# Optimization experiments

Hardware: AMD Instinct MI355X
Metric: run time of the kernel (lower is better)

Reference implementation:

```python
import jax, jax.numpy as jnp
import numpy as np
import math

BATCH, SEQ, DIM, HEADS = 2, 2048, 1024, 16
HD = DIM // HEADS  # 64
HID = int(DIM * 4 * 2 / 3)  # 2730


def cosine_norm(x):
    n = jnp.maximum(jnp.linalg.norm(x, axis=-1, keepdims=True), 1e-6)
    return x / n


def make_freqs(seq_len, head_dim, theta=10000.0):
    inv_freq = 1.0 / theta ** (jnp.arange(0, head_dim, 2, dtype=jnp.float32) / head_dim)
    t = jnp.arange(seq_len, dtype=jnp.float32)
    f = t[:, None] * inv_freq[None, :]            # [S, HD/2]
    emb = jnp.concatenate([f, f], axis=-1)        # [S, HD]
    return jnp.cos(emb)[None, :, None, :], jnp.sin(emb)[None, :, None, :]


def apply_rope(x, sin, cos):
    # x: [B, S, H, HD]
    x_real = x * cos
    x1, x2 = jnp.split(x, 2, axis=-1)
    x_imag = jnp.concatenate([-x2, x1], axis=-1) * sin
    return x_real + x_imag


def setup_inputs() -> dict:
    key = jax.random.key(0)
    ks = jax.random.split(key, 9)
    std = 0.02
    return {
        "x": jax.random.normal(ks[0], (BATCH, SEQ, DIM), dtype=jnp.float32),
        "Wq": jax.random.normal(ks[1], (DIM, DIM), dtype=jnp.float32) * std,
        "Wk": jax.random.normal(ks[2], (DIM, DIM), dtype=jnp.float32) * std,
        "Wv": jax.random.normal(ks[3], (DIM, DIM), dtype=jnp.float32) * std,
        "Wo": jax.random.normal(ks[4], (DIM, DIM), dtype=jnp.float32) * std,
        "s_qk": jnp.ones((HEADS, HD), dtype=jnp.float32) / math.sqrt(DIM),
        "a_A": jnp.ones((DIM,), dtype=jnp.float32) / math.sqrt(DIM),
        "Wup": jax.random.normal(ks[5], (DIM, HID), dtype=jnp.float32) * std,
        "Wgate": jax.random.normal(ks[6], (DIM, HID), dtype=jnp.float32) * std,
        "Wdown": jax.random.normal(ks[7], (HID, DIM), dtype=jnp.float32) * std,
        "s_u": jnp.ones((HID,), dtype=jnp.float32),
        "s_v": jnp.ones((HID,), dtype=jnp.float32),
        "a_M": jnp.ones((DIM,), dtype=jnp.float32) / math.sqrt(DIM),
    }


def attention(x, Wq, Wk, Wv, Wo, s_qk, cos, sin, mask):
    B, S, _ = x.shape
    q = (x @ Wq).reshape(B, S, HEADS, HD)
    k = (x @ Wk).reshape(B, S, HEADS, HD)
    v = (x @ Wv).reshape(B, S, HEADS, HD)
    q = apply_rope(q, sin, cos)
    k = apply_rope(k, sin, cos)
    eff_s_qk = s_qk * math.sqrt(DIM)  # s_qk_init / s_qk_scale = sqrt(dim)
    q = cosine_norm(q) * eff_s_qk
    k = cosine_norm(k) * eff_s_qk
    logits = jnp.einsum("bqhd,bkhd->bhqk", q, k) * math.sqrt(HD)
    logits = jnp.where(mask, logits, -jnp.inf)
    probs = jax.nn.softmax(logits, axis=-1)
    out = jnp.einsum("bhqk,bkhd->bqhd", probs, v).reshape(B, S, DIM)
    return out @ Wo


def mlp(x, Wup, Wgate, Wdown, s_u, s_v):
    u = (x @ Wup) * s_u                          # s_u_init/s_u_scale = 1
    v = (x @ Wgate) * s_v * math.sqrt(DIM)       # scale = sqrt(input_dim)
    return (u * jax.nn.silu(v)) @ Wdown


def reference(x, Wq, Wk, Wv, Wo, s_qk, a_A, Wup, Wgate, Wdown, s_u, s_v, a_M):
    cos, sin = make_freqs(SEQ, HD)
    mask = jnp.tril(jnp.ones((SEQ, SEQ), dtype=bool))[None, None, :, :]
    h = x
    h_A = cosine_norm(attention(h, Wq, Wk, Wv, Wo, s_qk, cos, sin, mask))
    h = cosine_norm(h + a_A * (h_A - h))
    h_M = cosine_norm(mlp(h, Wup, Wgate, Wdown, s_u, s_v))
    h = cosine_norm(h + a_M * (h_M - h))
    return h
```

## Files before the change

kernel.cpp:

```cpp
#include <hip/hip_runtime.h>
#include <math.h>

#define DEVI __device__ __forceinline__

typedef __attribute__((ext_vector_type(4))) float f32x4;
typedef __attribute__((ext_vector_type(8))) short bf16x8;

DEVI short f2bf(float f) {
    union { float f; unsigned u; } v; v.f = f;
    unsigned r = v.u + 0x7fffu + ((v.u >> 16) & 1u);
    return (short)(r >> 16);
}
DEVI float bf2f(short s) {
    union { unsigned u; float f; } v; v.u = ((unsigned)(unsigned short)s) << 16;
    return v.f;
}

DEVI f32x4 mfma16(bf16x8 a, bf16x8 b, f32x4 c) {
    return __builtin_amdgcn_mfma_f32_16x16x32_bf16(a, b, c, 0, 0, 0);
}

DEVI void gload16(const short* g, short* l) {
    __builtin_amdgcn_global_load_lds((__attribute__((address_space(1))) void*)(g),
                                     (__attribute__((address_space(3))) void*)(l),
                                     16, 0, 0);
}

DEVI void trans_tile(const float* in, short* out, int R, int C, int Rpad, int Cpad,
                     int rmul, int radd, int bx, int by) {
    __shared__ float tile[32][33];
    int c0 = bx * 32, r0 = by * 32;
    int tx = threadIdx.x & 31, ty = threadIdx.x >> 5;
#pragma unroll
    for (int i = 0; i < 4; i++) {
        int r = r0 + ty + 8 * i, c = c0 + tx;
        tile[ty + 8 * i][tx] = (r < R && c < C) ? in[(size_t)r * C + c] : 0.0f;
    }
    __syncthreads();
#pragma unroll
    for (int i = 0; i < 4; i++) {
        int oc = c0 + ty + 8 * i;
        int orr = r0 + tx;
        if (oc < Cpad && orr < Rpad)
            out[(size_t)(oc * rmul + radd) * Rpad + orr] = f2bf(tile[tx][ty + 8 * i]);
    }
}

__global__ void k_prep(const float* __restrict__ x, short* __restrict__ xbf,
                       float* __restrict__ cost, float* __restrict__ sint,
                       const float* __restrict__ Wq, const float* __restrict__ Wk,
                       const float* __restrict__ Wv, const float* __restrict__ Wo,
                       const float* __restrict__ Wup, const float* __restrict__ Wg,
                       const float* __restrict__ Wd,
                       short* __restrict__ wqkvT, short* __restrict__ woT,
                       short* __restrict__ wugT, short* __restrict__ wdownT) {
    int b = blockIdx.x;
    if (b < 4096) {
        int i = (b * 256 + threadIdx.x) * 4;
        float4 v = *(const float4*)(x + i);
        short4 o;
        o.x = f2bf(v.x); o.y = f2bf(v.y); o.z = f2bf(v.z); o.w = f2bf(v.w);
        *(short4*)(xbf + i) = o;
    } else if (b < 4352) {
        int i = (b - 4096) * 256 + threadIdx.x;
        int s = i >> 5, j = i & 31;
        double inv = pow(10000.0, -(double)j / 32.0);
        double f = (double)s * inv;
        cost[i] = (float)cos(f);
        sint[i] = (float)sin(f);
    } else {
        int bb = b - 4352;
        if (bb < 4096) {
            int seg = bb >> 10, idx = bb & 1023;
            const float* in = seg == 0 ? Wq : seg == 1 ? Wk : seg == 2 ? Wv : Wo;
            short* out = seg == 0 ? wqkvT : seg == 1 ? wqkvT + 1048576
                       : seg == 2 ? wqkvT + 2097152 : woT;
            trans_tile(in, out, 1024, 1024, 1024, 1024, 1, 0, idx & 31, idx >> 5);
        } else if (bb < 9600) {
            int idx = bb - 4096;
            int seg = idx >= 2752;
            idx -= seg * 2752;
            trans_tile(seg ? Wg : Wup, wugT, 1024, 2730, 1024, 2752, 2, seg, idx % 86, idx / 86);
        } else {
            int idx = bb - 9600;
            trans_tile(Wd, wdownT, 2730, 1024, 2752, 1024, 1, 0, idx & 31, idx >> 5);
        }
    }
}

template <int EPI>
__launch_bounds__(256, 4)
__global__ void k_gemm128(const short* __restrict__ A, const short* __restrict__ BT,
                          void* __restrict__ Cv, void* __restrict__ Cv1,
                          int M, int N, int K, int nkblk, int nsplit,
                          const float* __restrict__ s_u, const float* __restrict__ s_v,
                          const float* __restrict__ cost, const float* __restrict__ sint,
                          const float* __restrict__ sqk,
                          short* __restrict__ qn, short* __restrict__ kn,
                          short* __restrict__ vtout) {
    __shared__ __align__(16) short As[128 * 64];
    __shared__ __align__(16) short Bs[128 * 64];
    const int t = threadIdx.x;
    const int w = t >> 6;
    const int lane = t & 63;
    const int lr = lane & 15, lg = lane >> 4;
    const int nwg = (int)gridDim.x;
    int wg = ((int)blockIdx.x & 7) * (nwg >> 3) + ((int)blockIdx.x >> 3);
    int half = 0;
    if (nsplit == 2) {
        const int per = nwg >> 1;
        half = wg >= per;
        wg -= half * per;
    }
    const int MT = M >> 7;
    const int m0 = (wg % MT) << 7;
    const int n0 = (wg / MT) << 7;
    const int koff = half * nkblk * 64;
    const int ntile = (nsplit == 2 && half) ? (K >> 6) - nkblk : nkblk;
    const int wr = (w >> 1) * 64, wc = (w & 1) * 64;

    const int srow = t >> 3;
    const int scol = (((t & 7) ^ (srow & 7)) << 3);
    const short* Ap = A + (size_t)(m0 + srow) * K + koff + scol;
    const short* Bp = BT + (size_t)(n0 + srow) * K + koff + scol;
    const size_t rstep = (size_t)32 * K;
    const int dW = (w * 8) * 64;

    const int ca = (wr + lr) & 7;
    const int cb = (wc + lr) & 7;
    const short* pa0 = &As[(wr + lr) * 64 + (((0 + lg) ^ ca) << 3)];
    const short* pa1 = &As[(wr + lr) * 64 + (((4 + lg) ^ ca) << 3)];
    const short* pb0 = &Bs[(wc + lr) * 64 + (((0 + lg) ^ cb) << 3)];
    const short* pb1 = &Bs[(wc + lr) * 64 + (((4 + lg) ^ cb) << 3)];

    f32x4 acc[4][4];
#pragma unroll
    for (int m = 0; m < 4; m++)
#pragma unroll
        for (int n = 0; n < 4; n++)
            acc[m][n] = (f32x4){0.f, 0.f, 0.f, 0.f};

    for (int kt = 0; kt < ntile; kt++) {
        if (kt) __syncthreads();
#pragma unroll
        for (int j = 0; j < 4; j++) {
            gload16(Ap + j * rstep, As + dW + j * 2048);
            gload16(Bp + j * rstep, Bs + dW + j * 2048);
        }
        Ap += 64; Bp += 64;
        __syncthreads();
#pragma unroll
        for (int ks = 0; ks < 2; ks++) {
            const short* pa = ks ? pa1 : pa0;
            const short* pb = ks ? pb1 : pb0;
            bf16x8 af[4], bfr[4];
#pragma unroll
            for (int m = 0; m < 4; m++)
                af[m] = *(const bf16x8*)(pa + m * 1024);
#pragma unroll
            for (int n = 0; n < 4; n++)
                bfr[n] = *(const bf16x8*)(pb + n * 1024);
#pragma unroll
            for (int m = 0; m < 4; m++)
#pragma unroll
                for (int n = 0; n < 4; n++)
                    acc[m][n] = mfma16(af[m], bfr[n], acc[m][n]);
        }
    }

    if (EPI == 3) {
        const int sector = n0 >> 10;
        if (sector == 2) {
#pragma unroll
            for (int m = 0; m < 4; m++)
#pragma unroll
                for (int n = 0; n < 4; n++) {
                    int col = n0 + wc + n * 16 + lr - 2048;
                    int hh = col >> 6, d = col & 63;
                    int brow = m0 + wr + m * 16 + lg * 4;
                    int bb = brow >> 11, s = brow & 2047;
                    short4 o4;
                    o4.x = f2bf(acc[m][n][0]); o4.y = f2bf(acc[m][n][1]);
                    o4.z = f2bf(acc[m][n][2]); o4.w = f2bf(acc[m][n][3]);
                    *(short4*)&vtout[((size_t)((bb * 16 + hh) * 64 + d)) * 2048 + s] = o4;
                }
        } else {
            const int h = ((n0 + wc) >> 6) & 15;
            float eff[4];
#pragma unroll
            for (int n = 0; n < 4; n++)
                eff[n] = sqk[h * 64 + n * 16 + lr] * 32.0f;
            short* dst = (sector == 0) ? qn : kn;
            const float extra = (sector == 0) ? 8.0f : 1.0f;
#pragma unroll
            for (int m = 0; m < 4; m++)
#pragma unroll
                for (int i = 0; i < 4; i++) {
                    int row = m0 + wr + m * 16 + lg * 4 + i;
                    int b = row >> 11, s = row & 2047;
                    float cs0 = cost[s * 32 + lr],      sn0 = sint[s * 32 + lr];
                    float cs1 = cost[s * 32 + 16 + lr], sn1 = sint[s * 32 + 16 + lr];
                    float vr0 = acc[m][0][i] * cs0 - acc[m][2][i] * sn0;
                    float vr1 = acc[m][1][i] * cs1 - acc[m][3][i] * sn1;
                    float vr2 = acc[m][2][i] * cs0 + acc[m][0][i] * sn0;
                    float vr3 = acc[m][3][i] * cs1 + acc[m][1][i] * sn1;
                    float ss = vr0 * vr0 + vr1 * vr1 + vr2 * vr2 + vr3 * vr3;
#pragma unroll
                    for (int o = 1; o < 16; o <<= 1)
                        ss += __shfl_xor(ss, o, 64);
                    float sc = extra / fmaxf(sqrtf(ss), 1e-6f);
                    size_t base = ((size_t)(b * 16 + h) * 2048 + s) * 64;
                    dst[base + lr]      = f2bf(vr0 * eff[0] * sc);
                    dst[base + 16 + lr] = f2bf(vr1 * eff[1] * sc);
                    dst[base + 32 + lr] = f2bf(vr2 * eff[2] * sc);
                    dst[base + 48 + lr] = f2bf(vr3 * eff[3] * sc);
                }
        }
        return;
    }

#pragma unroll
    for (int m = 0; m < 4; m++)
#pragma unroll
        for (int n = 0; n < 4; n++) {
            int row = m0 + wr + m * 16 + lg * 4;
            int col = n0 + wc + n * 16 + lr;
            if (EPI == 2) {
                int j = col >> 1;
                int jc = j < 2730 ? j : 2729;
                float su = s_u[jc];
                float sg = s_v[jc] * 32.0f;
#pragma unroll
                for (int i = 0; i < 4; i++) {
                    float own = acc[m][n][i];
                    float oth = __shfl_xor(own, 1, 64);
                    float u = (lr & 1) ? oth : own;
                    float g = (lr & 1) ? own : oth;
                    float uu = u * su;
                    float vv = g * sg;
                    float wv = uu * vv / (1.0f + expf(-vv));
                    if (!(lr & 1))
                        ((short*)Cv)[(size_t)(row + i) * (N >> 1) + j] = f2bf(wv);
                }
            } else {
                void* outp = half ? Cv1 : Cv;
#pragma unroll
                for (int i = 0; i < 4; i++) {
                    if (EPI == 1)
                        ((short*)outp)[(size_t)(row + i) * N + col] = f2bf(acc[m][n][i]);
                    else
                        ((float*)outp)[(size_t)(row + i) * N + col] = acc[m][n][i];
                }
            }
        }
}

__launch_bounds__(512)
__global__ void k_attn(const short* __restrict__ qn, const short* __restrict__ kn,
                       const short* __restrict__ vt, short* __restrict__ opart,
                       float* __restrict__ lsump) {
    __shared__ __align__(16) short Ks[2][64 * 64];
    __shared__ __align__(16) short Vs[2][64 * 64];
    __shared__ __align__(16) short Ps[8][32 * 64];
    const int t = threadIdx.x;
    const int w = t >> 6, lane = t & 63;
    const int bid = blockIdx.x;
    const int xcd = bid & 7, idx = bid >> 3;
    const int bhg = xcd + ((idx >> 3) << 3);
    const int pslot = idx & 7;
    const int h = bhg & 15, b = bhg >> 4;
    const int bh = b * 16 + h;
    const int lr = lane & 15, lg = lane >> 4;
    const short* Qb = qn + (size_t)bh * 2048 * 64;
    const short* Kb = kn + (size_t)bh * 2048 * 64;
    const short* Vb = vt + (size_t)bh * 64 * 2048;
    char* pwc = (char*)&Ps[w][0];

#define STAGE_KV(bi, kbase)                                                          \
    {                                                                                \
        int row = w * 8 + (lane >> 3);                                               \
        int scol = (lane & 7) ^ (row & 7);                                           \
        gload16(Kb + (size_t)((kbase) + row) * 64 + scol * 8,                        \
                &Ks[bi][(w * 8) * 64]);                                              \
        gload16(Vb + (size_t)row * 2048 + (kbase) + scol * 8,                        \
                &Vs[bi][(w * 8) * 64]);                                              \
    }

    for (int pc = 0; pc < 2; pc++) {
        const int qb = pc == 0 ? pslot : 7 - pslot;
        const int hf = pc;
        const int ktn = 2 * qb + 2;
        const int kt0 = hf * ktn, kt1 = kt0 + ktn;
        const int qw = qb * 256 + w * 32;

        bf16x8 qf[2][2];
#pragma unroll
        for (int mi = 0; mi < 2; mi++)
#pragma unroll
            for (int kk = 0; kk < 2; kk++)
                qf[mi][kk] = *(const bf16x8*)&Qb[(size_t)(qw + mi * 16 + lr) * 64 + kk * 32 + lg * 8];

        f32x4 oacc[2][4];
#pragma unroll
        for (int mi = 0; mi < 2; mi++)
#pragma unroll
            for (int ct = 0; ct < 4; ct++) oacc[mi][ct] = (f32x4){0.f, 0.f, 0.f, 0.f};
        float psum[2][4];
#pragma unroll
        for (int mi = 0; mi < 2; mi++)
#pragma unroll
            for (int i = 0; i < 4; i++) psum[mi][i] = 0.0f;

        if (pc) __syncthreads();
        STAGE_KV(0, kt0 << 6);

        for (int kt = kt0; kt < kt1; kt++) {
            const int kbase = kt << 6;
            const int cur = (kt - kt0) & 1;
            __syncthreads();
            if (kt + 1 < kt1) STAGE_KV(cur ^ 1, (kt + 1) << 6);

            bf16x8 kf[4][2];
#pragma unroll
            for (int ni = 0; ni < 4; ni++)
#pragma unroll
                for (int kk = 0; kk < 2; kk++) {
                    int row = ni * 16 + lr;
                    kf[ni][kk] = *(const bf16x8*)&Ks[cur][row * 64 + (((kk * 4 + lg) ^ (row & 7)) << 3)];
                }
            f32x4 sv[2][4];
#pragma unroll
            for (int mi = 0; mi < 2; mi++)
#pragma unroll
                for (int ni = 0; ni < 4; ni++) {
                    f32x4 s = (f32x4){0.f, 0.f, 0.f, 0.f};
                    s = mfma16(qf[mi][0], kf[ni][0], s);
                    s = mfma16(qf[mi][1], kf[ni][1], s);
                    sv[mi][ni] = s;
                }
            if (kbase + 63 > qw) {
#pragma unroll
                for (int mi = 0; mi < 2; mi++)
#pragma unroll
                    for (int ni = 0; ni < 4; ni++)
#pragma unroll
                        for (int i = 0; i < 4; i++) {
                            int qg = qw + mi * 16 + lg * 4 + i;
                            int kg = kbase + ni * 16 + lr;
                            if (kg > qg) sv[mi][ni][i] = -3.0e38f;
                        }
            }
#pragma unroll
            for (int mi = 0; mi < 2; mi++) {
#pragma unroll
                for (int ni = 0; ni < 4; ni++)
#pragma unroll
                    for (int i = 0; i < 4; i++) {
                        float p = exp2f((sv[mi][ni][i] - 9.0f) * 1.44269504f);
                        sv[mi][ni][i] = p;
                        psum[mi][i] += p;
                    }
#pragma unroll
                for (int ni = 0; ni < 4; ni++)
#pragma unroll
                    for (int i = 0; i < 4; i++) {
                        int row = mi * 16 + lg * 4 + i;
                        int col = ni * 16 + lr;
                        unsigned off = (unsigned)(row * 128 + col * 2) ^ ((unsigned)(row & 7) << 4);
                        *(short*)(pwc + off) = f2bf(sv[mi][ni][i]);
                    }
            }
            bf16x8 pa[2][2];
#pragma unroll
            for (int mi = 0; mi < 2; mi++)
#pragma unroll
                for (int kk = 0; kk < 2; kk++) {
                    int row = mi * 16 + lr;
                    unsigned off = (unsigned)(row * 128 + kk * 64 + lg * 16) ^ ((unsigned)(row & 7) << 4);
                    pa[mi][kk] = *(const bf16x8*)(pwc + off);
                }
            bf16x8 vf[4][2];
#pragma unroll
            for (int ct = 0; ct < 4; ct++)
#pragma unroll
                for (int kk = 0; kk < 2; kk++) {
                    int row = ct * 16 + lr;
                    vf[ct][kk] = *(const bf16x8*)&Vs[cur][row * 64 + (((kk * 4 + lg) ^ (row & 7)) << 3)];
                }
#pragma unroll
            for (int mi = 0; mi < 2; mi++)
#pragma unroll
                for (int ct = 0; ct < 4; ct++) {
                    oacc[mi][ct] = mfma16(pa[mi][0], vf[ct][0], oacc[mi][ct]);
                    oacc[mi][ct] = mfma16(pa[mi][1], vf[ct][1], oacc[mi][ct]);
                }
        }

#pragma unroll
        for (int o = 1; o < 16; o <<= 1)
#pragma unroll
            for (int mi = 0; mi < 2; mi++)
#pragma unroll
                for (int i = 0; i < 4; i++)
                    psum[mi][i] += __shfl_xor(psum[mi][i], o, 64);

        short* aob = opart + (size_t)hf * 4096 * 1024 + ((size_t)(b * 2048 + qw) * 1024) + h * 64;
#pragma unroll
        for (int mi = 0; mi < 2; mi++)
#pragma unroll
            for (int ct = 0; ct < 4; ct++)
#pragma unroll
                for (int i = 0; i < 4; i++) {
                    int q = mi * 16 + lg * 4 + i;
                    aob[(size_t)q * 1024 + ct * 16 + lr] = f2bf(oacc[mi][ct][i]);
                }
        if (lr == 0) {
#pragma unroll
            for (int mi = 0; mi < 2; mi++)
#pragma unroll
                for (int i = 0; i < 4; i++)
                    lsump[hf * 65536 + bh * 2048 + qw + mi * 16 + lg * 4 + i] = psum[mi][i];
        }
    }
#undef STAGE_KV
}

__global__ void k_comb(const short* __restrict__ op, const float* __restrict__ ls,
                       short* __restrict__ ao) {
    int i = (blockIdx.x * 256 + threadIdx.x) * 4;
    int row = i >> 10, col = i & 1023;
    int idx = ((row >> 11) * 16 + (col >> 6)) * 2048 + (row & 2047);
    float rl = 1.0f / (ls[idx] + ls[65536 + idx]);
    short4 a = *(const short4*)(op + i);
    short4 c = *(const short4*)(op + 4194304 + i);
    short4 o;
    o.x = f2bf((bf2f(a.x) + bf2f(c.x)) * rl);
    o.y = f2bf((bf2f(a.y) + bf2f(c.y)) * rl);
    o.z = f2bf((bf2f(a.z) + bf2f(c.z)) * rl);
    o.w = f2bf((bf2f(a.w) + bf2f(c.w)) * rl);
    *(short4*)(ao + i) = o;
}

__global__ void k_resnorm(const float* base, const short* __restrict__ pre0,
                          const short* __restrict__ pre1,
                          const float* __restrict__ alpha, float* outf,
                          short* __restrict__ outb) {
    __shared__ float red1[4], red2[4];
    int row = blockIdx.x;
    int t = threadIdx.x;
    int w = t >> 6;
    float4 p;
    short4 a = *(const short4*)(pre0 + (size_t)row * 1024 + t * 4);
    short4 c = *(const short4*)(pre1 + (size_t)row * 1024 + t * 4);
    p.x = bf2f(a.x) + bf2f(c.x); p.y = bf2f(a.y) + bf2f(c.y);
    p.z = bf2f(a.z) + bf2f(c.z); p.w = bf2f(a.w) + bf2f(c.w);
    float ss = p.x * p.x + p.y * p.y + p.z * p.z + p.w * p.w;
#pragma unroll
    for (int o = 1; o < 64; o <<= 1) ss += __shfl_xor(ss, o, 64);
    if ((t & 63) == 0) red1[w] = ss;
    __syncthreads();
    float inv1 = 1.0f / fmaxf(sqrtf(red1[0] + red1[1] + red1[2] + red1[3]), 1e-6f);
    const float4 bx = *(const float4*)(base + (size_t)row * 1024 + t * 4);
    const float4 av = *(const float4*)(alpha + t * 4);
    float4 tm;
    tm.x = bx.x + av.x * (p.x * inv1 - bx.x);
    tm.y = bx.y + av.y * (p.y * inv1 - bx.y);
    tm.z = bx.z + av.z * (p.z * inv1 - bx.z);
    tm.w = bx.w + av.w * (p.w * inv1 - bx.w);
    float ss2 = tm.x * tm.x + tm.y * tm.y + tm.z * tm.z + tm.w * tm.w;
#pragma unroll
    for (int o = 1; o < 64; o <<= 1) ss2 += __shfl_xor(ss2, o, 64);
    if ((t & 63) == 0) red2[w] = ss2;
    __syncthreads();
    float inv2 = 1.0f / fmaxf(sqrtf(red2[0] + red2[1] + red2[2] + red2[3]), 1e-6f);
    float4 hv;
    hv.x = tm.x * inv2; hv.y = tm.y * inv2; hv.z = tm.z * inv2; hv.w = tm.w * inv2;
    if (outf) *(float4*)(outf + (size_t)row * 1024 + t * 4) = hv;
    if (outb) {
        short4 o4;
        o4.x = f2bf(hv.x); o4.y = f2bf(hv.y); o4.z = f2bf(hv.z); o4.w = f2bf(hv.w);
        *(short4*)(outb + (size_t)row * 1024 + t * 4) = o4;
    }
}

extern "C" void kernel_launch(void* const* d_in, const int* in_sizes, int n_in,
                              void* d_out, int out_size, void* d_ws, size_t ws_size,
                              hipStream_t stream) {
    (void)in_sizes; (void)n_in; (void)out_size; (void)ws_size;
    const float* x   = (const float*)d_in[0];
    const float* Wq  = (const float*)d_in[1];
    const float* Wk  = (const float*)d_in[2];
    const float* Wv  = (const float*)d_in[3];
    const float* Wo  = (const float*)d_in[4];
    const float* sqk = (const float*)d_in[5];
    const float* aA  = (const float*)d_in[6];
    const float* Wup = (const float*)d_in[7];
    const float* Wg  = (const float*)d_in[8];
    const float* Wd  = (const float*)d_in[9];
    const float* su  = (const float*)d_in[10];
    const float* sv  = (const float*)d_in[11];
    const float* aM  = (const float*)d_in[12];

    char* ws = (char*)d_ws;
    short* wqkvT  = (short*)(ws + 0);
    short* woT    = (short*)(ws + 6291456);
    short* wugT   = (short*)(ws + 8388608);
    short* wdownT = (short*)(ws + 19660800);
    float* cost   = (float*)(ws + 25296896);
    float* sint   = (float*)(ws + 25559040);
    short* xbf    = (short*)(ws + 25821184);
    short* qn     = (short*)(ws + 34209792);
    short* kn     = (short*)(ws + 42598400);
    short* vt     = (short*)(ws + 50987008);
    short* opart  = (short*)(ws + 59375616);
    float* lsum   = (float*)(ws + 25296896);
    short* ao     = (short*)(ws + 34209792);
    short* hA0    = (short*)(ws + 42598400);
    short* hA1    = (short*)(ws + 50987008);
    float* h1f    = (float*)d_out;
    short* h1bf   = (short*)(ws + 25821184);
    short* wmlp   = (short*)(ws + 34209792);
    short* hM0    = (short*)(ws + 59375616);
    short* hM1    = (short*)(ws + 67764224);

    k_prep<<<16704, 256, 0, stream>>>(x, xbf, cost, sint, Wq, Wk, Wv, Wo, Wup, Wg, Wd,
                                      wqkvT, woT, wugT, wdownT);

    k_gemm128<3><<<768, 256, 0, stream>>>(xbf, wqkvT, nullptr, nullptr, 4096, 3072, 1024,
                                          16, 1, nullptr, nullptr, cost, sint, sqk, qn, kn, vt);
    k_attn<<<256, 512, 0, stream>>>(qn, kn, vt, opart, lsum);
    k_comb<<<4096, 256, 0, stream>>>(opart, lsum, ao);
    k_gemm128<1><<<512, 256, 0, stream>>>(ao, woT, hA0, hA1, 4096, 1024, 1024,
                                          8, 2, nullptr, nullptr, nullptr, nullptr, nullptr,
                                          nullptr, nullptr, nullptr);
    k_resnorm<<<4096, 256, 0, stream>>>(x, hA0, hA1, aA, h1f, h1bf);
    k_gemm128<2><<<1376, 256, 0, stream>>>(h1bf, wugT, wmlp, nullptr, 4096, 5504, 1024,
                                           16, 1, su, sv, nullptr, nullptr, nullptr,
                                           nullptr, nullptr, nullptr);
    k_gemm128<1><<<512, 256, 0, stream>>>(wmlp, wdownT, hM0, hM1, 4096, 1024, 2752,
                                          22, 2, nullptr, nullptr, nullptr, nullptr, nullptr,
                                          nullptr, nullptr, nullptr);
    k_resnorm<<<4096, 256, 0, stream>>>(h1f, hM0, hM1, aM, (float*)d_out, (short*)nullptr);
}
```

Before: 241.1 us.

## Halve attention query tile per block and double grid size

The attention kernel now gives each wave 16 query rows instead of 32 and each block 128 queries instead of 256, so it launches 512 blocks rather than 256. The query block index ranges over 16 slots with pairing 15-pslot, which keeps causal work balanced across blocks, and the per-wave P scratch in shared memory is halved. The goal is more parallelism and occupancy across the CUs. In exchange, each K/V tile loaded into shared memory is reused by half as many queries, so K/V staging traffic and sync overhead per unit of work roughly double.

```diff
diff --git a/kernel.cpp b/kernel.cpp
--- a/kernel.cpp
+++ b/kernel.cpp
@@ -261,13 +261,13 @@
                        float* __restrict__ lsump) {
     __shared__ __align__(16) short Ks[2][64 * 64];
     __shared__ __align__(16) short Vs[2][64 * 64];
-    __shared__ __align__(16) short Ps[8][32 * 64];
+    __shared__ __align__(16) short Ps[8][16 * 64];
     const int t = threadIdx.x;
     const int w = t >> 6, lane = t & 63;
     const int bid = blockIdx.x;
     const int xcd = bid & 7, idx = bid >> 3;
-    const int bhg = xcd + ((idx >> 3) << 3);
-    const int pslot = idx & 7;
+    const int bhg = xcd + ((idx >> 4) << 3);
+    const int pslot = idx & 15;
     const int h = bhg & 15, b = bhg >> 4;
     const int bh = b * 16 + h;
     const int lr = lane & 15, lg = lane >> 4;
@@ -287,29 +287,21 @@
     }
 
     for (int pc = 0; pc < 2; pc++) {
-        const int qb = pc == 0 ? pslot : 7 - pslot;
+        const int qb = pc == 0 ? pslot : 15 - pslot;
         const int hf = pc;
-        const int ktn = 2 * qb + 2;
+        const int ktn = qb + 1;
         const int kt0 = hf * ktn, kt1 = kt0 + ktn;
-        const int qw = qb * 256 + w * 32;
-
-        bf16x8 qf[2][2];
-#pragma unroll
-        for (int mi = 0; mi < 2; mi++)
-#pragma unroll
-            for (int kk = 0; kk < 2; kk++)
-                qf[mi][kk] = *(const bf16x8*)&Qb[(size_t)(qw + mi * 16 + lr) * 64 + kk * 32 + lg * 8];
-
-        f32x4 oacc[2][4];
-#pragma unroll
-        for (int mi = 0; mi < 2; mi++)
-#pragma unroll
-            for (int ct = 0; ct < 4; ct++) oacc[mi][ct] = (f32x4){0.f, 0.f, 0.f, 0.f};
-        float psum[2][4];
-#pragma unroll
-        for (int mi = 0; mi < 2; mi++)
-#pragma unroll
-            for (int i = 0; i < 4; i++) psum[mi][i] = 0.0f;
+        const int qw = qb * 128 + w * 16;
+
+        bf16x8 qf[2];
+#pragma unroll
+        for (int kk = 0; kk < 2; kk++)
+            qf[kk] = *(const bf16x8*)&Qb[(size_t)(qw + lr) * 64 + kk * 32 + lg * 8];
+
+        f32x4 oacc[4];
+#pragma unroll
+        for (int ct = 0; ct < 4; ct++) oacc[ct] = (f32x4){0.f, 0.f, 0.f, 0.f};
+        float psum[4] = {0.f, 0.f, 0.f, 0.f};
 
         if (pc) __syncthreads();
         STAGE_KV(0, kt0 << 6);
@@ -328,57 +320,47 @@
                     int row = ni * 16 + lr;
                     kf[ni][kk] = *(const bf16x8*)&Ks[cur][row * 64 + (((kk * 4 + lg) ^ (row & 7)) << 3)];
                 }
-            f32x4 sv[2][4];
-#pragma unroll
-            for (int mi = 0; mi < 2; mi++)
-#pragma unroll
-                for (int ni = 0; ni < 4; ni++) {
-                    f32x4 s = (f32x4){0.f, 0.f, 0.f, 0.f};
-                    s = mfma16(qf[mi][0], kf[ni][0], s);
-                    s = mfma16(qf[mi][1], kf[ni][1], s);
-                    sv[mi][ni] = s;
-                }
+            f32x4 sv[4];
+#pragma unroll
+            for (int ni = 0; ni < 4; ni++) {
+                f32x4 s = (f32x4){0.f, 0.f, 0.f, 0.f};
+                s = mfma16(qf[0], kf[ni][0], s);
+                s = mfma16(qf[1], kf[ni][1], s);
+                sv[ni] = s;
+            }
             if (kbase + 63 > qw) {
 #pragma unroll
-                for (int mi = 0; mi < 2; mi++)
-#pragma unroll
-                    for (int ni = 0; ni < 4; ni++)
-#pragma unroll
-                        for (int i = 0; i < 4; i++) {
-                            int qg = qw + mi * 16 + lg * 4 + i;
-                            int kg = kbase + ni * 16 + lr;
-                            if (kg > qg) sv[mi][ni][i] = -3.0e38f;
-                        }
-            }
-#pragma unroll
-            for (int mi = 0; mi < 2; mi++) {
-#pragma unroll
                 for (int ni = 0; ni < 4; ni++)
 #pragma unroll
                     for (int i = 0; i < 4; i++) {
-                        float p = exp2f((sv[mi][ni][i] - 9.0f) * 1.44269504f);
-                        sv[mi][ni][i] = p;
-                        psum[mi][i] += p;
-                    }
-#pragma unroll
-                for (int ni = 0; ni < 4; ni++)
-#pragma unroll
-                    for (int i = 0; i < 4; i++) {
-                        int row = mi * 16 + lg * 4 + i;
-                        int col = ni * 16 + lr;
-                        unsigned off = (unsigned)(row * 128 + col * 2) ^ ((unsigned)(row & 7) << 4);
-                        *(short*)(pwc + off) = f2bf(sv[mi][ni][i]);
+                        int qg = qw + lg * 4 + i;
+                        int kg = kbase + ni * 16 + lr;
+                        if (kg > qg) sv[ni][i] = -3.0e38f;
                     }
             }
-            bf16x8 pa[2][2];
-#pragma unroll
-            for (int mi = 0; mi < 2; mi++)
-#pragma unroll
-                for (int kk = 0; kk < 2; kk++) {
-                    int row = mi * 16 + lr;
-                    unsigned off = (unsigned)(row * 128 + kk * 64 + lg * 16) ^ ((unsigned)(row & 7) << 4);
-                    pa[mi][kk] = *(const bf16x8*)(pwc + off);
-                }
+#pragma unroll
+            for (int ni = 0; ni < 4; ni++)
+#pragma unroll
+                for (int i = 0; i < 4; i++) {
+                    float p = exp2f((sv[ni][i] - 9.0f) * 1.44269504f);
+                    sv[ni][i] = p;
+                    psum[i] += p;
+                }
+#pragma unroll
+            for (int ni = 0; ni < 4; ni++)
+#pragma unroll
+                for (int i = 0; i < 4; i++) {
+                    int row = lg * 4 + i;
+                    int col = ni * 16 + lr;
+                    unsigned off = (unsigned)(row * 128 + col * 2) ^ ((unsigned)(row & 7) << 4);
+                    *(short*)(pwc + off) = f2bf(sv[ni][i]);
+                }
+            bf16x8 pa[2];
+#pragma unroll
+            for (int kk = 0; kk < 2; kk++) {
+                unsigned off = (unsigned)(lr * 128 + kk * 64 + lg * 16) ^ ((unsigned)(lr & 7) << 4);
+                pa[kk] = *(const bf16x8*)(pwc + off);
+            }
             bf16x8 vf[4][2];
 #pragma unroll
             for (int ct = 0; ct < 4; ct++)
@@ -388,38 +370,30 @@
                     vf[ct][kk] = *(const bf16x8*)&Vs[cur][row * 64 + (((kk * 4 + lg) ^ (row & 7)) << 3)];
                 }
 #pragma unroll
-            for (int mi = 0; mi < 2; mi++)
-#pragma unroll
-                for (int ct = 0; ct < 4; ct++) {
-                    oacc[mi][ct] = mfma16(pa[mi][0], vf[ct][0], oacc[mi][ct]);
-                    oacc[mi][ct] = mfma16(pa[mi][1], vf[ct][1], oacc[mi][ct]);
-                }
+            for (int ct = 0; ct < 4; ct++) {
+                oacc[ct] = mfma16(pa[0], vf[ct][0], oacc[ct]);
+                oacc[ct] = mfma16(pa[1], vf[ct][1], oacc[ct]);
+            }
         }
 
 #pragma unroll
         for (int o = 1; o < 16; o <<= 1)
 #pragma unroll
-            for (int mi = 0; mi < 2; mi++)
-#pragma unroll
-                for (int i = 0; i < 4; i++)
-                    psum[mi][i] += __shfl_xor(psum[mi][i], o, 64);
+            for (int i = 0; i < 4; i++)
+                psum[i] += __shfl_xor(psum[i], o, 64);
 
         short* aob = opart + (size_t)hf * 4096 * 1024 + ((size_t)(b * 2048 + qw) * 1024) + h * 64;
 #pragma unroll
-        for (int mi = 0; mi < 2; mi++)
-#pragma unroll
-            for (int ct = 0; ct < 4; ct++)
-#pragma unroll
-                for (int i = 0; i < 4; i++) {
-                    int q = mi * 16 + lg * 4 + i;
-                    aob[(size_t)q * 1024 + ct * 16 + lr] = f2bf(oacc[mi][ct][i]);
-                }
+        for (int ct = 0; ct < 4; ct++)
+#pragma unroll
+            for (int i = 0; i < 4; i++) {
+                int q = lg * 4 + i;
+                aob[(size_t)q * 1024 + ct * 16 + lr] = f2bf(oacc[ct][i]);
+            }
         if (lr == 0) {
 #pragma unroll
-            for (int mi = 0; mi < 2; mi++)
-#pragma unroll
-                for (int i = 0; i < 4; i++)
-                    lsump[hf * 65536 + bh * 2048 + qw + mi * 16 + lg * 4 + i] = psum[mi][i];
+            for (int i = 0; i < 4; i++)
+                lsump[hf * 65536 + bh * 2048 + qw + lg * 4 + i] = psum[i];
         }
     }
 #undef STAGE_KV
@@ -528,7 +502,7 @@
 
     k_gemm128<3><<<768, 256, 0, stream>>>(xbf, wqkvT, nullptr, nullptr, 4096, 3072, 1024,
                                           16, 1, nullptr, nullptr, cost, sint, sqk, qn, kn, vt);
-    k_attn<<<256, 512, 0, stream>>>(qn, kn, vt, opart, lsum);
+    k_attn<<<512, 512, 0, stream>>>(qn, kn, vt, opart, lsum);
     k_comb<<<4096, 256, 0, stream>>>(opart, lsum, ao);
     k_gemm128<1><<<512, 256, 0, stream>>>(ao, woT, hA0, hA1, 4096, 1024, 1024,
                                           8, 2, nullptr, nullptr, nullptr, nullptr, nullptr,
```

Result: faster. 232.1 us, median of 2 (-3.7%).
